# Kernel tuning notes

Measured on AMD Instinct MI355X. Metric: run time of the kernel, lower is better.

The kernel has to match this reference:

```python
import jax, jax.numpy as jnp
import numpy as np

B, A, S, U, H, E, HE, ACT = 16384, 8, 512, 64, 4, 64, 256, 16
REG_COEF = 0.001


def setup_inputs() -> dict:
    key = jax.random.key(0)
    ks = jax.random.split(key, 12)
    w = 0.02
    return {
        "agent_qs": jax.random.normal(ks[0], (B, A), jnp.float32),
        "states": jax.random.normal(ks[1], (B, A, S), jnp.float32),
        "actions": jax.random.normal(ks[2], (B, A, ACT), jnp.float32),
        # per-head selector hypernet: Linear(S,HE)+ReLU+Linear(HE,E,no bias)
        "sel_w1": jax.random.normal(ks[3], (H, S, HE), jnp.float32) * w,
        "sel_b1": jnp.zeros((H, HE), jnp.float32),
        "sel_w2": jax.random.normal(ks[4], (H, HE, E), jnp.float32) * w,
        # per-head key extractor: Linear(U,E,no bias)
        "key_w": jax.random.normal(ks[5], (H, U, E), jnp.float32) * w,
        # V net: Linear(S,E)+ReLU+Linear(E,1)
        "v_w1": jax.random.normal(ks[6], (S, E), jnp.float32) * w,
        "v_b1": jnp.zeros((E,), jnp.float32),
        "v_w2": jax.random.normal(ks[7], (E, 1), jnp.float32) * w,
        "v_b2": jnp.zeros((1,), jnp.float32),
    }


def reference(agent_qs, states, actions, sel_w1, sel_b1, sel_w2, key_w,
              v_w1, v_b1, v_w2, v_b2):
    # states.reshape(-1, A, S)[:, 0, :]
    st = states.reshape(-1, A, S)[:, 0, :]               # [B, S]
    unit = st[:, : U * A].reshape(-1, A, U)               # [B, A, U]
    # all heads at once: selector hypernet
    hmid = jax.nn.relu(jnp.einsum('bs,hsf->bhf', st, sel_w1) + sel_b1)  # [B,H,HE]
    sel = jnp.einsum('bhf,hfe->bhe', hmid, sel_w2)        # [B, H, E]
    keys = jnp.einsum('bau,hue->bhae', unit, key_w)       # [B, H, A, E]
    logits = jnp.einsum('bhe,bhae->bha', sel, keys)       # [B, H, A] (unscaled)
    weights = jax.nn.softmax(logits / np.sqrt(E).astype(np.float32), axis=-1)
    head_attend = jnp.sum(weights, axis=1)                # [B, A]
    v = jax.nn.relu(st @ v_w1 + v_b1) @ v_w2 + v_b2       # [B, 1]
    # sum over heads of mean(logits_h ** 2)
    attend_mag_regs = REG_COEF * jnp.sum(jnp.mean(logits ** 2, axis=(0, 2)))
    # per-head entropy: mean over batch of -sum_a p log(p+eps)
    head_entropies = -jnp.mean(
        jnp.sum(jnp.log(weights + 1e-8) * weights, axis=-1), axis=0)  # [H]
    return head_attend, v, attend_mag_regs, head_entropies
```

## Files before the change

### kernel.cpp

```cpp
#include <hip/hip_runtime.h>
#include <stdint.h>


typedef __attribute__((ext_vector_type(8))) short short8v;
typedef __attribute__((ext_vector_type(4))) float f32x4;

constexpr int BB = 16384, AA = 8, SS = 512, UU = 64, HH = 4, EE = 64, HE = 256;
constexpr int BT = 32;
constexpr int OUTV = BB * AA, OUTR = OUTV + BB, OUTE = OUTR + 1;

constexpr int OFF_W1F  = 0;
constexpr int OFF_W2F  = 524288;
constexpr int OFF_VW1F = 589824;
constexpr int OFF_KWF  = 622592;
constexpr int PREP_N   = 638976;

__device__ __forceinline__ unsigned short f2bf(float x) {
  union { float f; uint32_t u; } v; v.f = x;
  uint32_t r = v.u + 0x7fffu + ((v.u >> 16) & 1u);
  return (unsigned short)(r >> 16);
}
__device__ __forceinline__ float bf2f(short h) {
  union { uint32_t u; float f; } v; v.u = ((uint32_t)(unsigned short)h) << 16;
  return v.f;
}

__global__ __launch_bounds__(256) void prep_kernel(
    const float* __restrict__ w1, const float* __restrict__ w2,
    const float* __restrict__ vw1, const float* __restrict__ kw,
    unsigned short* __restrict__ ws) {
  int idx = blockIdx.x * 256 + threadIdx.x;
  if (idx >= PREP_N) return;
  int r = idx & 511, l = r >> 3, j = r & 7, lr = l & 15, g = l >> 4;
  int fi = idx >> 9;
  float val;
  if (idx < OFF_W2F) {
    int h = fi >> 8, tl = (fi >> 4) & 15, kf = fi & 15;
    int s = kf * 32 + g * 8 + j, f = tl * 16 + lr;
    val = w1[((size_t)(h * SS) + s) * HE + f];
  } else if (idx < OFF_VW1F) {
    fi -= OFF_W2F >> 9;
    int h = fi >> 5, tl = (fi >> 3) & 3, kf = fi & 7;
    int k = kf * 32 + g * 8 + j, e = tl * 16 + lr;
    val = w2[((size_t)(h * HE) + k) * EE + e];
  } else if (idx < OFF_KWF) {
    fi -= OFF_VW1F >> 9;
    int tl = fi >> 4, kf = fi & 15;
    int s = kf * 32 + g * 8 + j, e = tl * 16 + lr;
    val = vw1[(size_t)s * EE + e];
  } else {
    fi -= OFF_KWF >> 9;
    int h = fi >> 3, tl = (fi >> 1) & 3, kf = fi & 1;
    int k = kf * 32 + g * 8 + j, u = tl * 16 + lr;
    val = kw[((size_t)(h * UU) + u) * EE + k];
  }
  ws[idx] = f2bf(val);
}

__global__ __launch_bounds__(256) void qatten_mfma(
    const float* __restrict__ states, const float* __restrict__ sel_b1,
    const float* __restrict__ v_b1,  const float* __restrict__ v_w2,
    const float* __restrict__ v_b2,  const unsigned short* __restrict__ ws,
    float* __restrict__ out) {
  __shared__ __align__(16) unsigned char lds[63232];
  short* hmid = (short*)lds;
  short* sel  = (short*)(lds + 16896);
  short* stl  = (short*)lds;
  short* mm   = (short*)(lds + 33280);
  short* vhid = (short*)(lds + 50176);
  float* logitsL = (float*)(lds + 54784);
  float* wtsL    = (float*)(lds + 59008);

  const int t  = threadIdx.x;
  const int w  = t >> 6, l = t & 63;
  const int mt = w & 1, nh = w >> 1;
  const int lr = l & 15, g = l >> 4;
  const int b0 = blockIdx.x * BT;
  const short* w1f  = (const short*)ws + OFF_W1F;
  const short* w2f  = (const short*)ws + OFF_W2F;
  const short* vw1f = (const short*)ws + OFF_VW1F;
  const short* kwf  = (const short*)ws + OFF_KWF;

  short8v aF[16];
  {
    const float* srow = states + (size_t)(b0 + mt * 16 + lr) * (AA * SS);
    #pragma unroll
    for (int f = 0; f < 16; ++f) {
      float4 p0 = *(const float4*)(srow + f * 32 + g * 8);
      float4 p1 = *(const float4*)(srow + f * 32 + g * 8 + 4);
      short8v a;
      a[0] = (short)f2bf(p0.x); a[1] = (short)f2bf(p0.y);
      a[2] = (short)f2bf(p0.z); a[3] = (short)f2bf(p0.w);
      a[4] = (short)f2bf(p1.x); a[5] = (short)f2bf(p1.y);
      a[6] = (short)f2bf(p1.z); a[7] = (short)f2bf(p1.w);
      aF[f] = a;
    }
  }

  for (int h = 0; h < HH; ++h) {
    f32x4 acc[8] = {{0,0,0,0},{0,0,0,0},{0,0,0,0},{0,0,0,0},
                    {0,0,0,0},{0,0,0,0},{0,0,0,0},{0,0,0,0}};
    {
      const short* bb = w1f + ((size_t)(h * 256 + nh * 128)) * 512 + l * 8;
      #pragma unroll
      for (int kf = 0; kf < 16; ++kf) {
        short8v af = aF[kf];
        #pragma unroll
        for (int tl = 0; tl < 8; ++tl)
          acc[tl] = __builtin_amdgcn_mfma_f32_16x16x32_bf16(
              af, *(const short8v*)(bb + (size_t)(tl * 16 + kf) * 512),
              acc[tl], 0, 0, 0);
      }
    }
    #pragma unroll
    for (int tl = 0; tl < 8; ++tl) {
      int fb = (nh * 8 + tl) * 16;
      float bias = sel_b1[h * HE + fb + lr];
      #pragma unroll
      for (int r2 = 0; r2 < 4; ++r2)
        hmid[(mt * 16 + g * 4 + r2) * 264 + fb + lr] =
            (short)f2bf(fmaxf(acc[tl][r2] + bias, 0.f));
    }
    __syncthreads();

    f32x4 a2[2] = {{0,0,0,0},{0,0,0,0}};
    {
      const short* ah = hmid + (mt * 16 + lr) * 264 + g * 8;
      const short* b2 = w2f + ((size_t)(h * 32 + nh * 16)) * 512 + l * 8;
      #pragma unroll
      for (int kf = 0; kf < 8; ++kf) {
        short8v af = *(const short8v*)(ah + kf * 32);
        #pragma unroll
        for (int tl = 0; tl < 2; ++tl)
          a2[tl] = __builtin_amdgcn_mfma_f32_16x16x32_bf16(
              af, *(const short8v*)(b2 + (size_t)(tl * 8 + kf) * 512),
              a2[tl], 0, 0, 0);
      }
    }
    #pragma unroll
    for (int tl = 0; tl < 2; ++tl)
      #pragma unroll
      for (int r2 = 0; r2 < 4; ++r2)
        sel[(mt * 16 + g * 4 + r2) * 72 + (nh * 2 + tl) * 16 + lr] =
            (short)f2bf(a2[tl][r2]);
    __syncthreads();

    f32x4 a3[2] = {{0,0,0,0},{0,0,0,0}};
    {
      const short* as = sel + (mt * 16 + lr) * 72 + g * 8;
      const short* b3 = kwf + ((size_t)(h * 8 + nh * 4)) * 512 + l * 8;
      #pragma unroll
      for (int kf = 0; kf < 2; ++kf) {
        short8v af = *(const short8v*)(as + kf * 32);
        #pragma unroll
        for (int tl = 0; tl < 2; ++tl)
          a3[tl] = __builtin_amdgcn_mfma_f32_16x16x32_bf16(
              af, *(const short8v*)(b3 + (size_t)(tl * 2 + kf) * 512),
              a3[tl], 0, 0, 0);
      }
    }
    #pragma unroll
    for (int tl = 0; tl < 2; ++tl)
      #pragma unroll
      for (int r2 = 0; r2 < 4; ++r2)
        mm[(mt * 16 + g * 4 + r2) * 264 + h * 64 + (nh * 2 + tl) * 16 + lr] =
            (short)f2bf(a3[tl][r2]);
    __syncthreads();
  }

  {
    f32x4 av[2] = {{0,0,0,0},{0,0,0,0}};
    const short* bv = vw1f + ((size_t)(nh * 32)) * 512 + l * 8;
    #pragma unroll
    for (int kf = 0; kf < 16; ++kf) {
      short8v af = aF[kf];
      #pragma unroll
      for (int tl = 0; tl < 2; ++tl)
        av[tl] = __builtin_amdgcn_mfma_f32_16x16x32_bf16(
            af, *(const short8v*)(bv + (size_t)(tl * 16 + kf) * 512),
            av[tl], 0, 0, 0);
    }
    #pragma unroll
    for (int tl = 0; tl < 2; ++tl) {
      int eb = (nh * 2 + tl) * 16;
      float bias = v_b1[eb + lr];
      #pragma unroll
      for (int r2 = 0; r2 < 4; ++r2)
        vhid[(mt * 16 + g * 4 + r2) * 72 + eb + lr] =
            (short)f2bf(fmaxf(av[tl][r2] + bias, 0.f));
    }
  }
  __syncthreads();

  {
    int b = t >> 3, r = t & 7;
    short8v hv = *(const short8v*)(vhid + b * 72 + r * 8);
    float p = 0.f;
    #pragma unroll
    for (int j = 0; j < 8; ++j) p += bf2f(hv[j]) * v_w2[r * 8 + j];
    p += __shfl_xor(p, 1); p += __shfl_xor(p, 2); p += __shfl_xor(p, 4);
    if (r == 0) out[OUTV + b0 + b] = p + v_b2[0];
  }
  if (w < 2) {
    #pragma unroll
    for (int f = 0; f < 16; ++f)
      *(short8v*)(stl + (w * 16 + lr) * 520 + f * 32 + g * 8) = aF[f];
  }
  __syncthreads();

  #pragma unroll
  for (int i = 0; i < 4; ++i) {
    int o = t + 256 * i;
    int b = o >> 5, hh = (o >> 3) & 3, a = o & 7;
    float lg = 0.f;
    #pragma unroll
    for (int j = 0; j < 8; ++j) {
      short8v s8 = *(const short8v*)(stl + b * 520 + a * 64 + j * 8);
      short8v m8 = *(const short8v*)(mm + b * 264 + hh * 64 + j * 8);
      #pragma unroll
      for (int q = 0; q < 8; ++q) lg += bf2f(s8[q]) * bf2f(m8[q]);
    }
    logitsL[b * 33 + hh * 8 + a] = lg;
  }
  __syncthreads();

  if (t < 128) {
    int b = t >> 2, hh = t & 3;
    float sc[8];
    float rp = 0.f, mx = -1e30f;
    #pragma unroll
    for (int a = 0; a < 8; ++a) {
      float lg = logitsL[b * 33 + hh * 8 + a];
      rp += lg * lg;
      sc[a] = lg * 0.125f;
      mx = fmaxf(mx, sc[a]);
    }
    float sum = 0.f;
    #pragma unroll
    for (int a = 0; a < 8; ++a) { sc[a] = __expf(sc[a] - mx); sum += sc[a]; }
    float inv = 1.f / sum, ent = 0.f;
    #pragma unroll
    for (int a = 0; a < 8; ++a) {
      float wv = sc[a] * inv;
      wtsL[b * 33 + hh * 8 + a] = wv;
      ent += wv * __logf(wv + 1e-8f);
    }
    #pragma unroll
    for (int off = 1; off <= 32; off <<= 1) rp += __shfl_xor(rp, off);
    if ((t & 63) == 0)
      atomicAdd(out + OUTR, rp * (0.001f / ((float)BB * (float)AA)));
    float ep = ent;
    #pragma unroll
    for (int off = 4; off <= 32; off <<= 1) ep += __shfl_xor(ep, off);
    if ((t & 63) < 4) atomicAdd(out + OUTE + hh, -ep / (float)BB);
  }
  __syncthreads();
  {
    int b = t >> 3, a = t & 7;
    out[(size_t)(b0 + b) * AA + a] = wtsL[b * 33 + a] + wtsL[b * 33 + 8 + a] +
                                     wtsL[b * 33 + 16 + a] + wtsL[b * 33 + 24 + a];
  }
}

extern "C" void kernel_launch(void* const* d_in, const int* in_sizes, int n_in,
                              void* d_out, int out_size, void* d_ws, size_t ws_size,
                              hipStream_t stream) {
  (void)in_sizes; (void)n_in; (void)ws_size; (void)out_size;
  const float* states = (const float*)d_in[1];
  const float* sel_w1 = (const float*)d_in[3];
  const float* sel_b1 = (const float*)d_in[4];
  const float* sel_w2 = (const float*)d_in[5];
  const float* key_w  = (const float*)d_in[6];
  const float* v_w1   = (const float*)d_in[7];
  const float* v_b1   = (const float*)d_in[8];
  const float* v_w2   = (const float*)d_in[9];
  const float* v_b2   = (const float*)d_in[10];
  float* out = (float*)d_out;
  unsigned short* ws = (unsigned short*)d_ws;

  hipMemsetAsync(out + OUTR, 0, 5 * sizeof(float), stream);
  prep_kernel<<<(PREP_N + 255) / 256, 256, 0, stream>>>(sel_w1, sel_w2, v_w1,
                                                        key_w, ws);
  qatten_mfma<<<BB / BT, 256, 0, stream>>>(states, sel_b1, v_b1, v_w2, v_b2,
                                           ws, out);
}
```

Baseline: 117.0 us.

## Compute logits per head from register state fragments, shrink LDS for occupancy

Logit dot products are now computed inside the per-head loop, straight from the state fragments already held in registers. A cross-lane shuffle reduction replaces the pass that staged the states tile and the full per-head key matrix in LDS. This cuts the LDS footprint from about 63KB to about 39KB, and launch_bounds now requests 3 blocks per CU to use the freed space for occupancy. The cost is extra shuffles and scalar bf16 multiply-adds inside the head loop, plus tighter register limits that may cause spills given the 16 short8v fragments kept live.

Result: slower. 194.4 us (+66.1%).

```diff
diff --git a/kernel.cpp b/kernel.cpp
--- a/kernel.cpp
+++ b/kernel.cpp
@@ -57,19 +57,18 @@
   ws[idx] = f2bf(val);
 }
 
-__global__ __launch_bounds__(256) void qatten_mfma(
+__global__ __launch_bounds__(256, 3) void qatten_mfma(
     const float* __restrict__ states, const float* __restrict__ sel_b1,
     const float* __restrict__ v_b1,  const float* __restrict__ v_w2,
     const float* __restrict__ v_b2,  const unsigned short* __restrict__ ws,
     float* __restrict__ out) {
-  __shared__ __align__(16) unsigned char lds[63232];
+  __shared__ __align__(16) unsigned char lds[39168];
   short* hmid = (short*)lds;
   short* sel  = (short*)(lds + 16896);
-  short* stl  = (short*)lds;
-  short* mm   = (short*)(lds + 33280);
-  short* vhid = (short*)(lds + 50176);
-  float* logitsL = (float*)(lds + 54784);
-  float* wtsL    = (float*)(lds + 59008);
+  short* mh   = (short*)(lds + 21504);
+  short* vhid = (short*)(lds + 26112);
+  float* logitsL = (float*)(lds + 30720);
+  float* wtsL    = (float*)(lds + 34944);
 
   const int t  = threadIdx.x;
   const int w  = t >> 6, l = t & 63;
@@ -163,9 +162,27 @@
     for (int tl = 0; tl < 2; ++tl)
       #pragma unroll
       for (int r2 = 0; r2 < 4; ++r2)
-        mm[(mt * 16 + g * 4 + r2) * 264 + h * 64 + (nh * 2 + tl) * 16 + lr] =
+        mh[(mt * 16 + g * 4 + r2) * 72 + (nh * 2 + tl) * 16 + lr] =
             (short)f2bf(a3[tl][r2]);
     __syncthreads();
+
+    {
+      const short* mrow = mh + (mt * 16 + lr) * 72;
+      short8v mv0 = *(const short8v*)(mrow + g * 8);
+      short8v mv1 = *(const short8v*)(mrow + 32 + g * 8);
+      #pragma unroll
+      for (int ai = 0; ai < 4; ++ai) {
+        int a = nh * 4 + ai;
+        short8v a0 = aF[a * 2], a1 = aF[a * 2 + 1];
+        float p = 0.f;
+        #pragma unroll
+        for (int j = 0; j < 8; ++j)
+          p += bf2f(a0[j]) * bf2f(mv0[j]) + bf2f(a1[j]) * bf2f(mv1[j]);
+        p += __shfl_xor(p, 16);
+        p += __shfl_xor(p, 32);
+        if (g == 0) logitsL[(mt * 16 + lr) * 33 + h * 8 + a] = p;
+      }
+    }
   }
 
   {
@@ -200,27 +217,6 @@
     for (int j = 0; j < 8; ++j) p += bf2f(hv[j]) * v_w2[r * 8 + j];
     p += __shfl_xor(p, 1); p += __shfl_xor(p, 2); p += __shfl_xor(p, 4);
     if (r == 0) out[OUTV + b0 + b] = p + v_b2[0];
-  }
-  if (w < 2) {
-    #pragma unroll
-    for (int f = 0; f < 16; ++f)
-      *(short8v*)(stl + (w * 16 + lr) * 520 + f * 32 + g * 8) = aF[f];
-  }
-  __syncthreads();
-
-  #pragma unroll
-  for (int i = 0; i < 4; ++i) {
-    int o = t + 256 * i;
-    int b = o >> 5, hh = (o >> 3) & 3, a = o & 7;
-    float lg = 0.f;
-    #pragma unroll
-    for (int j = 0; j < 8; ++j) {
-      short8v s8 = *(const short8v*)(stl + b * 520 + a * 64 + j * 8);
-      short8v m8 = *(const short8v*)(mm + b * 264 + hh * 64 + j * 8);
-      #pragma unroll
-      for (int q = 0; q < 8; ++q) lg += bf2f(s8[q]) * bf2f(m8[q]);
-    }
-    logitsL[b * 33 + hh * 8 + a] = lg;
   }
   __syncthreads();
 
```
